# Optimization experiments

Measured on AMD Instinct MI355X. Metric: run time of the kernel, lower is better.

The kernel has to match this reference:

```python
import jax, jax.numpy as jnp
import numpy as np

N = 131072   # total nodes
E = 1048576  # total edges
F = 32       # node_feature_dim
H = 128      # hidden_dim
G = 512      # num_graphs
MAX_NEURONS = 1000
NUM_ACTIONS = 5
NUM_ACTIVATIONS = 4


def setup_inputs() -> dict:
    key = jax.random.key(0)
    ks = jax.random.split(key, 16)
    xavier = lambda k, fi, fo: jax.random.uniform(k, (fi, fo), jnp.float32,
                                                  -np.sqrt(6.0 / (fi + fo)), np.sqrt(6.0 / (fi + fo)))
    return {
        'node_features': jax.random.normal(ks[0], (1, N, F), jnp.float32),
        'edge_index': jax.random.randint(ks[1], (2, E), 0, N, jnp.int64),
        'edge_weights': jax.random.uniform(ks[2], (E,), jnp.float32),
        'layer_positions': jax.random.randint(ks[3], (1, N), 0, 16, jnp.int64),
        'batch': jnp.sort(jax.random.randint(ks[4], (N,), 0, G, jnp.int64)),
        'num_graphs': G,
        'W_in': xavier(ks[5], F, H),
        'W_msg': xavier(ks[6], H, H),
        'W1': xavier(ks[7], 2 * H, H),
        'W2': xavier(ks[8], H, H // 2),
        'Wa': xavier(ks[9], H // 2, NUM_ACTIONS),
        'Ws': xavier(ks[10], H // 2, MAX_NEURONS),
        'Wt': xavier(ks[11], H // 2, MAX_NEURONS),
        'Wact': xavier(ks[12], H // 2, NUM_ACTIVATIONS),
        'Wv1': xavier(ks[13], H // 2, H // 4),
        'Wv2': xavier(ks[14], H // 4, 1),
    }


def reference(node_features, edge_index, edge_weights, layer_positions, batch, num_graphs,
              W_in, W_msg, W1, W2, Wa, Ws, Wt, Wact, Wv1, Wv2):
    # GraphTransformer node encoder: project + one edge-weighted message pass
    h0 = jnp.einsum('bnf,fh->nh', node_features, W_in)  # [N,H]
    src, tgt = edge_index[0], edge_index[1]
    msg = jax.ops.segment_sum(h0[src] * edge_weights[:, None], tgt, num_segments=h0.shape[0])
    h = jax.nn.relu(h0 + msg @ W_msg)  # node_embeddings [N,H]

    # per-graph masked mean pool (branch: sub_batch_size >= num_graphs)
    seg = jax.ops.segment_sum(h, batch, num_segments=num_graphs)           # [G,H]
    cnt = jax.ops.segment_sum(jnp.ones((h.shape[0], 1), h.dtype), batch, num_segments=num_graphs)
    g = jnp.where(cnt > 0, seg / jnp.maximum(cnt, 1.0), 0.0)
    ge = jnp.concatenate([g, g], axis=-1)  # torch.cat([emb, emb], -1) -> [G,2H]

    # shared backbone (dropout is identity at eval)
    s = jax.nn.relu(ge @ W1)
    s = jax.nn.relu(s @ W2)  # [G,H//2]

    action_type = s @ Wa
    source_logits = s @ Ws
    target_logits = s @ Wt
    activation_logits = s @ Wact
    value = jnp.tanh(jax.nn.relu(s @ Wv1) @ Wv2)
    return (action_type, source_logits, target_logits, activation_logits, value)
```

## Files before the change

kernel.cpp:

```cpp
#include <hip/hip_runtime.h>
#include <math.h>

#define NODES   131072
#define EDGES   1048576
#define FDIM    32
#define HDIM    128
#define NGRAPH  512

#define NB      256
#define BSH     9
#define MAXPER  5120
#define EPB     4096

typedef __attribute__((ext_vector_type(8))) short short8v;
typedef __attribute__((ext_vector_type(4))) float float4v;
typedef __attribute__((ext_vector_type(2))) float float2v;

__device__ __forceinline__ unsigned short f2bf(float f) {
    union { float f; unsigned int u; } v; v.f = f;
    unsigned int u = v.u;
    unsigned int r = (u + 0x7fffu + ((u >> 16) & 1u)) >> 16;
    return (unsigned short)r;
}

__device__ __forceinline__ void dec8(uint2 r, float* o) {
    float2v a = __builtin_amdgcn_cvt_pk_f32_fp8((int)r.x, false);
    float2v b = __builtin_amdgcn_cvt_pk_f32_fp8((int)r.x, true);
    float2v c = __builtin_amdgcn_cvt_pk_f32_fp8((int)r.y, false);
    float2v d = __builtin_amdgcn_cvt_pk_f32_fp8((int)r.y, true);
    o[0] = a.x; o[1] = a.y; o[2] = b.x; o[3] = b.y;
    o[4] = c.x; o[5] = c.y; o[6] = d.x; o[7] = d.y;
}

__global__ __launch_bounds__(256) void k1_fused(const float* __restrict__ x,
                                                const unsigned short* __restrict__ winfrag,
                                                unsigned char* __restrict__ h0f8,
                                                const int* __restrict__ ei,
                                                const float* __restrict__ ew,
                                                int* __restrict__ coarse_cursor,
                                                uint2* __restrict__ scratch) {
    __shared__ __align__(16) uint2 recL[EPB];
    __shared__ unsigned char bidL[EPB];
    __shared__ int hist[NB];
    __shared__ int excl[NB];
    __shared__ int gb[NB];

    int b = blockIdx.x, t = threadIdx.x;

    if (b < NB) {
        int e0 = b * EPB;
        hist[t] = 0;
        __syncthreads();

        unsigned int rx[16], rw[16];
        int bb[16], lr[16];
#pragma unroll
        for (int i = 0; i < 16; ++i) {
            int e = e0 + t + 256 * i;
            int src = ei[e];
            int tgt = ei[EDGES + e];
            float w = ew[e];
            int bk = tgt >> BSH;
            rx[i] = (unsigned int)src | ((unsigned int)(tgt & ((1 << BSH) - 1)) << 17);
            rw[i] = __float_as_uint(w);
            bb[i] = bk;
            lr[i] = atomicAdd(&hist[bk], 1);
        }
        __syncthreads();

        int hv = hist[t];
        excl[t] = hv;
        __syncthreads();
        for (int off = 1; off < 256; off <<= 1) {
            int v = (t >= off) ? excl[t - off] : 0;
            __syncthreads();
            excl[t] += v;
            __syncthreads();
        }
        int ex = excl[t] - hv;
        gb[t] = atomicAdd(&coarse_cursor[t], hv);
        __syncthreads();
        excl[t] = ex;
        __syncthreads();

#pragma unroll
        for (int i = 0; i < 16; ++i) {
            int pos = excl[bb[i]] + lr[i];
            recL[pos] = make_uint2(rx[i], rw[i]);
            bidL[pos] = (unsigned char)bb[i];
        }
        __syncthreads();

#pragma unroll
        for (int i = 0; i < 16; ++i) {
            int p2 = t + 256 * i;
            int bk = bidL[p2];
            int dst = bk * MAXPER + gb[bk] + (p2 - excl[bk]);
            scratch[dst] = recL[p2];
        }
    } else {
        int mb = b - NB;
        int wid = t >> 6, l = t & 63;
        int base = mb * 128;

        const short8v* wf8 = (const short8v*)winfrag;
        short8v wfr[8];
#pragma unroll
        for (int c = 0; c < 8; ++c) wfr[c] = wf8[c * 64 + l];

#pragma unroll
        for (int s = 0; s < 2; ++s) {
            int strip = base + wid * 32 + s * 16;
            int row = strip + (l & 15);
            const float* xr = x + (size_t)row * FDIM + (l >> 4) * 8;
            float4 x0 = ((const float4*)xr)[0];
            float4 x1 = ((const float4*)xr)[1];
            short8v af;
            af[0] = (short)f2bf(x0.x); af[1] = (short)f2bf(x0.y);
            af[2] = (short)f2bf(x0.z); af[3] = (short)f2bf(x0.w);
            af[4] = (short)f2bf(x1.x); af[5] = (short)f2bf(x1.y);
            af[6] = (short)f2bf(x1.z); af[7] = (short)f2bf(x1.w);

            float4v acc[8];
#pragma unroll
            for (int c = 0; c < 8; ++c) acc[c] = (float4v){0.f, 0.f, 0.f, 0.f};
#pragma unroll
            for (int c = 0; c < 8; ++c)
                acc[c] = __builtin_amdgcn_mfma_f32_16x16x32_bf16(af, wfr[c], acc[c], 0, 0, 0);

            int rbase = strip + (l >> 4) * 4;
            int m = l & 15;
#pragma unroll
            for (int r = 0; r < 4; ++r) {
                int w0 = __builtin_amdgcn_cvt_pk_fp8_f32(acc[0][r], acc[1][r], 0, false);
                w0     = __builtin_amdgcn_cvt_pk_fp8_f32(acc[2][r], acc[3][r], w0, true);
                int w1 = __builtin_amdgcn_cvt_pk_fp8_f32(acc[4][r], acc[5][r], 0, false);
                w1     = __builtin_amdgcn_cvt_pk_fp8_f32(acc[6][r], acc[7][r], w1, true);
                *((uint2*)(h0f8 + (size_t)(rbase + r) * HDIM + m * 8)) = make_uint2((unsigned)w0, (unsigned)w1);
            }
        }
    }
}

__global__ __launch_bounds__(256) void kp2_fine(const uint2* __restrict__ scratch,
                                                const int* __restrict__ coarse_cursor,
                                                int2* __restrict__ nbe,
                                                int2* __restrict__ csre) {
    __shared__ int fh[512];
    __shared__ int ts[256];
    __shared__ int ccs[256];

    int b = blockIdx.x, t = threadIdx.x;

    ccs[t] = coarse_cursor[t];
    fh[t] = 0; fh[t + 256] = 0;
    __syncthreads();
    for (int off = 1; off < 256; off <<= 1) {
        int v = (t >= off) ? ccs[t - off] : 0;
        __syncthreads();
        ccs[t] += v;
        __syncthreads();
    }
    int gbase = (b > 0) ? ccs[b - 1] : 0;
    int cnt_b = coarse_cursor[b];
    const uint2* src = scratch + (size_t)b * MAXPER;

    for (int j = t; j < cnt_b; j += 256) {
        uint2 r = src[j];
        atomicAdd(&fh[r.x >> 17], 1);
    }
    __syncthreads();

    int c0 = fh[2 * t], c1 = fh[2 * t + 1];
    int s = c0 + c1;
    ts[t] = s;
    __syncthreads();
    for (int off = 1; off < 256; off <<= 1) {
        int v = (t >= off) ? ts[t - off] : 0;
        __syncthreads();
        ts[t] += v;
        __syncthreads();
    }
    int tb = gbase + ts[t] - s;

    nbe[b * 512 + 2 * t]     = make_int2(tb, tb + c0);
    nbe[b * 512 + 2 * t + 1] = make_int2(tb + c0, tb + c0 + c1);
    __syncthreads();
    fh[2 * t] = tb; fh[2 * t + 1] = tb + c0;
    __syncthreads();

    for (int j = t; j < cnt_b; j += 256) {
        uint2 r = src[j];
        int pos = atomicAdd(&fh[r.x >> 17], 1);
        csre[pos] = make_int2((int)(r.x & 0x1FFFFu), (int)r.y);
    }
}

__global__ __launch_bounds__(256) void kprep(const float* __restrict__ Wmsg,
                                             const float* __restrict__ Win,
                                             unsigned short* __restrict__ wfrag,
                                             unsigned short* __restrict__ winfrag,
                                             const int* __restrict__ batch,
                                             int* __restrict__ cnt,
                                             float* __restrict__ gsum,
                                             int* __restrict__ coarse_cursor) {
    int b = blockIdx.x, t = threadIdx.x;
    if (b < 8) {
        int flat = b * 256 + t;
        int l = flat & 63;
        int fragid = flat >> 6;
        int c = fragid >> 2, kk = fragid & 3;
        int col = c * 16 + (l & 15);
        short8v v;
#pragma unroll
        for (int j = 0; j < 8; ++j) {
            int q = kk * 32 + (l >> 4) * 8 + j;
            int krow = (q & 7) * 16 + (q >> 3);
            v[j] = (short)f2bf(Wmsg[krow * HDIM + col]);
        }
        ((short8v*)wfrag)[flat] = v;
    } else if (b < 10) {
        int flat = (b - 8) * 256 + t;
        int l = flat & 63;
        int c = flat >> 6;
        int col = c * 16 + (l & 15);
        int k0 = (l >> 4) * 8;
        short8v v;
#pragma unroll
        for (int j = 0; j < 8; ++j)
            v[j] = (short)f2bf(Win[(k0 + j) * HDIM + col]);
        ((short8v*)winfrag)[flat] = v;
    } else if (b < 12) {
        int g = (b - 10) * 256 + t;
        if (g < NGRAPH) {
            int lo = 0, hi = NODES;
            while (lo < hi) { int m = (lo + hi) >> 1; if (batch[m] < g) lo = m + 1; else hi = m; }
            int start = lo;
            hi = NODES;
            while (lo < hi) { int m = (lo + hi) >> 1; if (batch[m] < g + 1) lo = m + 1; else hi = m; }
            cnt[g] = lo - start;
        }
    } else if (b < 14) {
        float4* gz = (float4*)gsum;
        int idx = (b - 12) * 256 + t;
        for (int i = idx; i < 16384; i += 512) gz[i] = make_float4(0.f, 0.f, 0.f, 0.f);
    } else {
        coarse_cursor[t] = 0;
    }
}

#define ACC8(r, w) do { \
    float2v q01 = __builtin_amdgcn_cvt_pk_f32_fp8((int)(r).x, false); \
    float2v q23 = __builtin_amdgcn_cvt_pk_f32_fp8((int)(r).x, true);  \
    float2v q45 = __builtin_amdgcn_cvt_pk_f32_fp8((int)(r).y, false); \
    float2v q67 = __builtin_amdgcn_cvt_pk_f32_fp8((int)(r).y, true);  \
    acc0 = fmaf(q01.x, (w), acc0); acc1 = fmaf(q01.y, (w), acc1); \
    acc2 = fmaf(q23.x, (w), acc2); acc3 = fmaf(q23.y, (w), acc3); \
    acc4 = fmaf(q45.x, (w), acc4); acc5 = fmaf(q45.y, (w), acc5); \
    acc6 = fmaf(q67.x, (w), acc6); acc7 = fmaf(q67.y, (w), acc7); \
} while (0)

__global__ __launch_bounds__(256) void kg_gather(const unsigned char* __restrict__ h0f8,
                                                 const int2* __restrict__ nbe,
                                                 const int2* __restrict__ csre,
                                                 unsigned short* __restrict__ msgb, int N) {
    int t = threadIdx.x;
    int wid = t >> 6, l = t & 63;
    int grp = l >> 4, m = l & 15;
    int n = blockIdx.x * 16 + wid * 4 + grp;

    int2 be = nbe[n];
    int j = be.x, end = be.y;
    float acc0 = 0.f, acc1 = 0.f, acc2 = 0.f, acc3 = 0.f;
    float acc4 = 0.f, acc5 = 0.f, acc6 = 0.f, acc7 = 0.f;

    for (; j + 4 <= end; j += 4) {
        int2 e0 = csre[j], e1 = csre[j + 1], e2 = csre[j + 2], e3 = csre[j + 3];
        uint2 r0 = ((const uint2*)(h0f8 + (size_t)e0.x * HDIM))[m];
        uint2 r1 = ((const uint2*)(h0f8 + (size_t)e1.x * HDIM))[m];
        uint2 r2 = ((const uint2*)(h0f8 + (size_t)e2.x * HDIM))[m];
        uint2 r3 = ((const uint2*)(h0f8 + (size_t)e3.x * HDIM))[m];
        float w0 = __int_as_float(e0.y), w1 = __int_as_float(e1.y);
        float w2 = __int_as_float(e2.y), w3 = __int_as_float(e3.y);
        ACC8(r0, w0); ACC8(r1, w1); ACC8(r2, w2); ACC8(r3, w3);
    }
    for (; j < end; ++j) {
        int2 e0 = csre[j];
        uint2 r0 = ((const uint2*)(h0f8 + (size_t)e0.x * HDIM))[m];
        float w0 = __int_as_float(e0.y);
        ACC8(r0, w0);
    }

    short8v v;
    v[0] = (short)f2bf(acc0); v[1] = (short)f2bf(acc1);
    v[2] = (short)f2bf(acc2); v[3] = (short)f2bf(acc3);
    v[4] = (short)f2bf(acc4); v[5] = (short)f2bf(acc5);
    v[6] = (short)f2bf(acc6); v[7] = (short)f2bf(acc7);
    ((short8v*)(msgb + (size_t)n * HDIM))[m] = v;
}

__global__ __launch_bounds__(256) void k3a_mfma_pool(const unsigned short* __restrict__ msgb,
                                                     const unsigned char* __restrict__ h0f8,
                                                     const unsigned short* __restrict__ wfrag,
                                                     const int* __restrict__ batch,
                                                     float* __restrict__ gsum) {
    __shared__ __align__(16) unsigned short blds[32 * 64 * 8];
    __shared__ float pool[8][HDIM];
    __shared__ int batch_lds[128];

    int t = threadIdx.x;
    int wid = t >> 6, l = t & 63;
    int base = blockIdx.x * 128;

    {
        const uint4* sp = (const uint4*)wfrag;
        uint4* d = (uint4*)blds;
#pragma unroll
        for (int i = 0; i < 8; ++i) d[t + 256 * i] = sp[t + 256 * i];
    }
    if (t < 128) batch_lds[t] = batch[base + t];
    __syncthreads();

    int bfirst = batch_lds[0];
    int blast  = batch_lds[127];
    int span = blast - bfirst + 1;

    const short8v* Bl = (const short8v*)blds;
    int col = l & 15;

    if (span <= 2) {
        float pa[8], pb[8];
#pragma unroll
        for (int c = 0; c < 8; ++c) { pa[c] = 0.f; pb[c] = 0.f; }

#pragma unroll
        for (int s = 0; s < 2; ++s) {
            int strip = base + wid * 32 + s * 16;
            const short8v* mrow = (const short8v*)(msgb + (size_t)(strip + col) * HDIM);
            short8v af[4];
#pragma unroll
            for (int kk = 0; kk < 4; ++kk) af[kk] = mrow[kk * 4 + (l >> 4)];
            int rbase = strip + (l >> 4) * 4;
            uint2 h8[4];
#pragma unroll
            for (int r = 0; r < 4; ++r)
                h8[r] = *((const uint2*)(h0f8 + (size_t)(rbase + r) * HDIM + col * 8));

            float4v acc[8];
#pragma unroll
            for (int c = 0; c < 8; ++c) acc[c] = (float4v){0.f, 0.f, 0.f, 0.f};
#pragma unroll
            for (int kk = 0; kk < 4; ++kk)
#pragma unroll
                for (int c = 0; c < 8; ++c)
                    acc[c] = __builtin_amdgcn_mfma_f32_16x16x32_bf16(af[kk], Bl[(c * 4 + kk) * 64 + l], acc[c], 0, 0, 0);

#pragma unroll
            for (int r = 0; r < 4; ++r) {
                bool isA = (batch_lds[rbase + r - base] == bfirst);
                float h0v[8];
                dec8(h8[r], h0v);
#pragma unroll
                for (int c = 0; c < 8; ++c) {
                    float hv = fmaxf(h0v[c] + acc[c][r], 0.f);
                    pa[c] += isA ? hv : 0.f;
                    pb[c] += isA ? 0.f : hv;
                }
            }
        }
#pragma unroll
        for (int c = 0; c < 8; ++c) {
            pa[c] += __shfl_xor(pa[c], 16);
            pa[c] += __shfl_xor(pa[c], 32);
            pb[c] += __shfl_xor(pb[c], 16);
            pb[c] += __shfl_xor(pb[c], 32);
        }
        float (*p2)[2][HDIM] = (float (*)[2][HDIM])pool;
        if (l < 16) {
#pragma unroll
            for (int c = 0; c < 8; ++c) {
                p2[wid][0][c * 16 + l] = pa[c];
                p2[wid][1][c * 16 + l] = pb[c];
            }
        }
        __syncthreads();
        int cc2 = t & 127, sidx = t >> 7;
        if (sidx < span) {
            float v = p2[0][sidx][cc2] + p2[1][sidx][cc2] + p2[2][sidx][cc2] + p2[3][sidx][cc2];
            atomicAdd(&gsum[(size_t)(bfirst + sidx) * HDIM + cc2], v);
        }
    } else {
        bool lds_pool = (span <= 8);
        if (lds_pool) {
            float* pf = (float*)pool;
            for (int i = t; i < 8 * HDIM; i += 256) pf[i] = 0.f;
        }
        __syncthreads();

#pragma unroll
        for (int s = 0; s < 2; ++s) {
            int strip = base + wid * 32 + s * 16;
            const short8v* mrow = (const short8v*)(msgb + (size_t)(strip + col) * HDIM);
            short8v af[4];
#pragma unroll
            for (int kk = 0; kk < 4; ++kk) af[kk] = mrow[kk * 4 + (l >> 4)];
            int rbase = strip + (l >> 4) * 4;
            uint2 h8[4];
#pragma unroll
            for (int r = 0; r < 4; ++r)
                h8[r] = *((const uint2*)(h0f8 + (size_t)(rbase + r) * HDIM + col * 8));

            float4v acc[8];
#pragma unroll
            for (int c = 0; c < 8; ++c) acc[c] = (float4v){0.f, 0.f, 0.f, 0.f};
#pragma unroll
            for (int kk = 0; kk < 4; ++kk)
#pragma unroll
                for (int c = 0; c < 8; ++c)
                    acc[c] = __builtin_amdgcn_mfma_f32_16x16x32_bf16(af[kk], Bl[(c * 4 + kk) * 64 + l], acc[c], 0, 0, 0);

            if (lds_pool) {
#pragma unroll
                for (int r = 0; r < 4; ++r) {
                    int g = batch_lds[rbase + r - base] - bfirst;
                    float h0v[8];
                    dec8(h8[r], h0v);
#pragma unroll
                    for (int c = 0; c < 8; ++c) {
                        float hv = fmaxf(h0v[c] + acc[c][r], 0.f);
                        atomicAdd(&pool[g][c * 16 + col], hv);
                    }
                }
            } else {
#pragma unroll
                for (int r = 0; r < 4; ++r) {
                    int g = batch_lds[rbase + r - base];
                    float h0v[8];
                    dec8(h8[r], h0v);
#pragma unroll
                    for (int c = 0; c < 8; ++c) {
                        float hv = fmaxf(h0v[c] + acc[c][r], 0.f);
                        atomicAdd(&gsum[(size_t)g * HDIM + c * 16 + col], hv);
                    }
                }
            }
        }
        __syncthreads();
        if (lds_pool) {
            int cc2 = t & 127;
            for (int s2 = t >> 7; s2 < span; s2 += 2)
                atomicAdd(&gsum[(size_t)(bfirst + s2) * HDIM + cc2], pool[s2][cc2]);
        }
    }
}

__global__ __launch_bounds__(128) void k4a_backbone(const float* __restrict__ gsum,
                                                    const int* __restrict__ cnt,
                                                    const float* __restrict__ W1,
                                                    const float* __restrict__ W2,
                                                    const float* __restrict__ Wv1,
                                                    const float* __restrict__ Wv2,
                                                    float* __restrict__ s2g,
                                                    float* __restrict__ out) {
    int g = blockIdx.x;
    int t = threadIdx.x;
    __shared__ float gv[HDIM];
    __shared__ float s1[HDIM];
    __shared__ float s2v[64];
    __shared__ float v1[32];

    {
        int c = cnt[g];
        gv[t] = (c > 0) ? gsum[(size_t)g * HDIM + t] / (float)c : 0.f;
    }
    __syncthreads();

    {
        float s = 0.f;
#pragma unroll 8
        for (int k = 0; k < HDIM; ++k)
            s = fmaf(gv[k], W1[k * HDIM + t] + W1[(k + HDIM) * HDIM + t], s);
        s1[t] = fmaxf(s, 0.f);
    }
    __syncthreads();

    if (t < 64) {
        float s = 0.f;
#pragma unroll 8
        for (int k = 0; k < HDIM; ++k)
            s = fmaf(s1[k], W2[k * 64 + t], s);
        float sv = fmaxf(s, 0.f);
        s2v[t] = sv;
        s2g[(size_t)g * 64 + t] = sv;
    }
    __syncthreads();

    if (t < 32) {
        float s = 0.f;
#pragma unroll 8
        for (int k = 0; k < 64; ++k)
            s = fmaf(s2v[k], Wv1[k * 32 + t], s);
        v1[t] = fmaxf(s, 0.f);
    }
    __syncthreads();
    if (t == 0) {
        float s = 0.f;
#pragma unroll
        for (int k = 0; k < 32; ++k)
            s = fmaf(v1[k], Wv2[k], s);
        out[1028608 + (size_t)g] = tanhf(s);
    }
}

__global__ __launch_bounds__(256) void k4b_logits(const float* __restrict__ s2g,
                                                  const float* __restrict__ Wa,
                                                  const float* __restrict__ Ws,
                                                  const float* __restrict__ Wt,
                                                  const float* __restrict__ Wact,
                                                  float* __restrict__ out) {
    int ctile = blockIdx.x & 7;
    int gbase = (blockIdx.x >> 3) * 16;
    int t = threadIdx.x;
    int col = ctile * 256 + t;

    __shared__ float4 s2s4[16][16];
    {
        int g = t >> 4, q = t & 15;
        s2s4[g][q] = ((const float4*)(s2g + (size_t)(gbase + g) * 64))[q];
    }

    bool valid = (col < 2009);
    const float* W = Wa; int colc = 0, ncol = 5; size_t hb = 0;
    if (col < 5)        { W = Wa;   colc = col;        ncol = 5;    hb = 0; }
    else if (col < 1005){ W = Ws;   colc = col - 5;    ncol = 1000; hb = 2560; }
    else if (col < 2005){ W = Wt;   colc = col - 1005; ncol = 1000; hb = 514560; }
    else                { W = Wact; colc = col - 2005; ncol = 4;    hb = 1026560; }

    float wr[64];
#pragma unroll
    for (int k = 0; k < 64; ++k)
        wr[k] = valid ? W[(size_t)k * ncol + colc] : 0.f;
    __syncthreads();

    for (int gg = 0; gg < 16; ++gg) {
        const float4* s4 = (const float4*)s2s4[gg];
        float a = 0.f;
#pragma unroll
        for (int q = 0; q < 16; ++q) {
            float4 v = s4[q];
            a = fmaf(v.x, wr[4 * q + 0], a);
            a = fmaf(v.y, wr[4 * q + 1], a);
            a = fmaf(v.z, wr[4 * q + 2], a);
            a = fmaf(v.w, wr[4 * q + 3], a);
        }
        if (valid) out[hb + (size_t)(gbase + gg) * ncol + colc] = a;
    }
}

extern "C" void kernel_launch(void* const* d_in, const int* in_sizes, int n_in,
                              void* d_out, int out_size, void* d_ws, size_t ws_size,
                              hipStream_t stream) {
    const float* x     = (const float*)d_in[0];
    const int*   ei    = (const int*)d_in[1];
    const float* ew    = (const float*)d_in[2];
    const int*   batch = (const int*)d_in[4];
    const float* Win   = (const float*)d_in[6];
    const float* Wmsg  = (const float*)d_in[7];
    const float* W1    = (const float*)d_in[8];
    const float* W2    = (const float*)d_in[9];
    const float* Wa    = (const float*)d_in[10];
    const float* Ws    = (const float*)d_in[11];
    const float* Wt    = (const float*)d_in[12];
    const float* Wact  = (const float*)d_in[13];
    const float* Wv1   = (const float*)d_in[14];
    const float* Wv2   = (const float*)d_in[15];
    float* out = (float*)d_out;

    char* p = (char*)d_ws;
    const size_t nb = (size_t)NODES * HDIM * 2;
    unsigned char*  h0f8   = (unsigned char*)p;   p += (size_t)NODES * HDIM;
    unsigned short* msgb   = (unsigned short*)p;  p += nb;
    float*          gsum   = (float*)p;           p += (size_t)NGRAPH * HDIM * 4;
    float*          s2g    = (float*)p;           p += (size_t)NGRAPH * 64 * 4;
    unsigned short* wfrag  = (unsigned short*)p;  p += 32 * 64 * 16;
    unsigned short* winfrag= (unsigned short*)p;  p += 8 * 64 * 16;
    int*            cnt    = (int*)p;             p += (size_t)NGRAPH * 4;
    int*            ccur   = (int*)p;             p += NB * 4;
    uint2*          scratch= (uint2*)p;           p += (size_t)NB * MAXPER * 8;
    int2*           nbe    = (int2*)p;            p += (size_t)NODES * 8;
    int2*           csre   = (int2*)p;            p += (size_t)EDGES * 8;

    kprep        <<<15, 256, 0, stream>>>(Wmsg, Win, wfrag, winfrag, batch, cnt, gsum, ccur);
    k1_fused     <<<NB + 1024, 256, 0, stream>>>(x, winfrag, h0f8, ei, ew, ccur, scratch);
    kp2_fine     <<<NB, 256, 0, stream>>>(scratch, ccur, nbe, csre);

    kg_gather    <<<NODES / 16, 256, 0, stream>>>(h0f8, nbe, csre, msgb, NODES);

    k3a_mfma_pool<<<NODES / 128, 256, 0, stream>>>(msgb, h0f8, wfrag, batch, gsum);

    k4a_backbone <<<NGRAPH, 128, 0, stream>>>(gsum, cnt, W1, W2, Wv1, Wv2, s2g, out);
    k4b_logits   <<<256, 256, 0, stream>>>(s2g, Wa, Ws, Wt, Wact, out);
}
```

Before: 113.0 us.

## Fuse CSR gather into MFMA pool kernel, staging messages in LDS

Merges the neighbor-gather kernel into the MFMA/pooling kernel. Each block first gathers the aggregated messages for its 128 nodes into a padded LDS tile, then runs the MFMA and pooling reading operands from LDS. This removes the bf16 message buffer round trip through global memory (a 32 MB write plus re-read) and one kernel launch. In exchange, LDS use grows by about 35 KB per block, which may lower occupancy. The gather is also now spread over 1024 blocks instead of 8192, cutting latency hiding for the irregular loads.

```diff
diff --git a/kernel.cpp b/kernel.cpp
--- a/kernel.cpp
+++ b/kernel.cpp
@@ -260,51 +260,16 @@
     acc6 = fmaf(q67.x, (w), acc6); acc7 = fmaf(q67.y, (w), acc7); \
 } while (0)
 
-__global__ __launch_bounds__(256) void kg_gather(const unsigned char* __restrict__ h0f8,
+#define MROW 136
+
+__global__ __launch_bounds__(256) void k3b_fused(const unsigned char* __restrict__ h0f8,
                                                  const int2* __restrict__ nbe,
                                                  const int2* __restrict__ csre,
-                                                 unsigned short* __restrict__ msgb, int N) {
-    int t = threadIdx.x;
-    int wid = t >> 6, l = t & 63;
-    int grp = l >> 4, m = l & 15;
-    int n = blockIdx.x * 16 + wid * 4 + grp;
-
-    int2 be = nbe[n];
-    int j = be.x, end = be.y;
-    float acc0 = 0.f, acc1 = 0.f, acc2 = 0.f, acc3 = 0.f;
-    float acc4 = 0.f, acc5 = 0.f, acc6 = 0.f, acc7 = 0.f;
-
-    for (; j + 4 <= end; j += 4) {
-        int2 e0 = csre[j], e1 = csre[j + 1], e2 = csre[j + 2], e3 = csre[j + 3];
-        uint2 r0 = ((const uint2*)(h0f8 + (size_t)e0.x * HDIM))[m];
-        uint2 r1 = ((const uint2*)(h0f8 + (size_t)e1.x * HDIM))[m];
-        uint2 r2 = ((const uint2*)(h0f8 + (size_t)e2.x * HDIM))[m];
-        uint2 r3 = ((const uint2*)(h0f8 + (size_t)e3.x * HDIM))[m];
-        float w0 = __int_as_float(e0.y), w1 = __int_as_float(e1.y);
-        float w2 = __int_as_float(e2.y), w3 = __int_as_float(e3.y);
-        ACC8(r0, w0); ACC8(r1, w1); ACC8(r2, w2); ACC8(r3, w3);
-    }
-    for (; j < end; ++j) {
-        int2 e0 = csre[j];
-        uint2 r0 = ((const uint2*)(h0f8 + (size_t)e0.x * HDIM))[m];
-        float w0 = __int_as_float(e0.y);
-        ACC8(r0, w0);
-    }
-
-    short8v v;
-    v[0] = (short)f2bf(acc0); v[1] = (short)f2bf(acc1);
-    v[2] = (short)f2bf(acc2); v[3] = (short)f2bf(acc3);
-    v[4] = (short)f2bf(acc4); v[5] = (short)f2bf(acc5);
-    v[6] = (short)f2bf(acc6); v[7] = (short)f2bf(acc7);
-    ((short8v*)(msgb + (size_t)n * HDIM))[m] = v;
-}
-
-__global__ __launch_bounds__(256) void k3a_mfma_pool(const unsigned short* __restrict__ msgb,
-                                                     const unsigned char* __restrict__ h0f8,
-                                                     const unsigned short* __restrict__ wfrag,
-                                                     const int* __restrict__ batch,
-                                                     float* __restrict__ gsum) {
+                                                 const unsigned short* __restrict__ wfrag,
+                                                 const int* __restrict__ batch,
+                                                 float* __restrict__ gsum) {
     __shared__ __align__(16) unsigned short blds[32 * 64 * 8];
+    __shared__ __align__(16) unsigned short msgL[128][MROW];
     __shared__ float pool[8][HDIM];
     __shared__ int batch_lds[128];
 
@@ -319,6 +284,40 @@
         for (int i = 0; i < 8; ++i) d[t + 256 * i] = sp[t + 256 * i];
     }
     if (t < 128) batch_lds[t] = batch[base + t];
+
+    {
+        int grp = l >> 4, m = l & 15;
+#pragma unroll
+        for (int pass = 0; pass < 8; ++pass) {
+            int nl = pass * 16 + wid * 4 + grp;
+            int2 be = nbe[base + nl];
+            int j = be.x, end = be.y;
+            float acc0 = 0.f, acc1 = 0.f, acc2 = 0.f, acc3 = 0.f;
+            float acc4 = 0.f, acc5 = 0.f, acc6 = 0.f, acc7 = 0.f;
+            for (; j + 4 <= end; j += 4) {
+                int2 e0 = csre[j], e1 = csre[j + 1], e2 = csre[j + 2], e3 = csre[j + 3];
+                uint2 r0 = ((const uint2*)(h0f8 + (size_t)e0.x * HDIM))[m];
+                uint2 r1 = ((const uint2*)(h0f8 + (size_t)e1.x * HDIM))[m];
+                uint2 r2 = ((const uint2*)(h0f8 + (size_t)e2.x * HDIM))[m];
+                uint2 r3 = ((const uint2*)(h0f8 + (size_t)e3.x * HDIM))[m];
+                float w0 = __int_as_float(e0.y), w1 = __int_as_float(e1.y);
+                float w2 = __int_as_float(e2.y), w3 = __int_as_float(e3.y);
+                ACC8(r0, w0); ACC8(r1, w1); ACC8(r2, w2); ACC8(r3, w3);
+            }
+            for (; j < end; ++j) {
+                int2 e0 = csre[j];
+                uint2 r0 = ((const uint2*)(h0f8 + (size_t)e0.x * HDIM))[m];
+                float w0 = __int_as_float(e0.y);
+                ACC8(r0, w0);
+            }
+            short8v v;
+            v[0] = (short)f2bf(acc0); v[1] = (short)f2bf(acc1);
+            v[2] = (short)f2bf(acc2); v[3] = (short)f2bf(acc3);
+            v[4] = (short)f2bf(acc4); v[5] = (short)f2bf(acc5);
+            v[6] = (short)f2bf(acc6); v[7] = (short)f2bf(acc7);
+            *((short8v*)&msgL[nl][m * 8]) = v;
+        }
+    }
     __syncthreads();
 
     int bfirst = batch_lds[0];
@@ -335,12 +334,12 @@
 
 #pragma unroll
         for (int s = 0; s < 2; ++s) {
-            int strip = base + wid * 32 + s * 16;
-            const short8v* mrow = (const short8v*)(msgb + (size_t)(strip + col) * HDIM);
+            int lrow = wid * 32 + s * 16 + col;
             short8v af[4];
 #pragma unroll
-            for (int kk = 0; kk < 4; ++kk) af[kk] = mrow[kk * 4 + (l >> 4)];
-            int rbase = strip + (l >> 4) * 4;
+            for (int kk = 0; kk < 4; ++kk)
+                af[kk] = *((const short8v*)&msgL[lrow][(kk * 4 + (l >> 4)) * 8]);
+            int rbase = base + wid * 32 + s * 16 + (l >> 4) * 4;
             uint2 h8[4];
 #pragma unroll
             for (int r = 0; r < 4; ++r)
@@ -399,12 +398,12 @@
 
 #pragma unroll
         for (int s = 0; s < 2; ++s) {
-            int strip = base + wid * 32 + s * 16;
-            const short8v* mrow = (const short8v*)(msgb + (size_t)(strip + col) * HDIM);
+            int lrow = wid * 32 + s * 16 + col;
             short8v af[4];
 #pragma unroll
-            for (int kk = 0; kk < 4; ++kk) af[kk] = mrow[kk * 4 + (l >> 4)];
-            int rbase = strip + (l >> 4) * 4;
+            for (int kk = 0; kk < 4; ++kk)
+                af[kk] = *((const short8v*)&msgL[lrow][(kk * 4 + (l >> 4)) * 8]);
+            int rbase = base + wid * 32 + s * 16 + (l >> 4) * 4;
             uint2 h8[4];
 #pragma unroll
             for (int r = 0; r < 4; ++r)
@@ -577,9 +576,7 @@
     float* out = (float*)d_out;
 
     char* p = (char*)d_ws;
-    const size_t nb = (size_t)NODES * HDIM * 2;
     unsigned char*  h0f8   = (unsigned char*)p;   p += (size_t)NODES * HDIM;
-    unsigned short* msgb   = (unsigned short*)p;  p += nb;
     float*          gsum   = (float*)p;           p += (size_t)NGRAPH * HDIM * 4;
     float*          s2g    = (float*)p;           p += (size_t)NGRAPH * 64 * 4;
     unsigned short* wfrag  = (unsigned short*)p;  p += 32 * 64 * 16;
@@ -594,9 +591,7 @@
     k1_fused     <<<NB + 1024, 256, 0, stream>>>(x, winfrag, h0f8, ei, ew, ccur, scratch);
     kp2_fine     <<<NB, 256, 0, stream>>>(scratch, ccur, nbe, csre);
 
-    kg_gather    <<<NODES / 16, 256, 0, stream>>>(h0f8, nbe, csre, msgb, NODES);
-
-    k3a_mfma_pool<<<NODES / 128, 256, 0, stream>>>(msgb, h0f8, wfrag, batch, gsum);
+    k3b_fused    <<<NODES / 128, 256, 0, stream>>>(h0f8, nbe, csre, wfrag, batch, gsum);
 
     k4a_backbone <<<NGRAPH, 128, 0, stream>>>(gsum, cnt, W1, W2, Wv1, Wv2, s2g, out);
     k4b_logits   <<<256, 256, 0, stream>>>(s2g, Wa, Ws, Wt, Wact, out);
```

Result: slower. 142.0 us (+25.7%).
